# Optimization experiments

Hardware: AMD Instinct MI355X
Metric: run time of the kernel (lower is better)

Reference implementation:

```python
import jax, jax.numpy as jnp
import numpy as np


def setup_inputs() -> dict:
    key = jax.random.key(0)
    k1, k2, k3, k4, k5 = jax.random.split(key, 5)
    B, S, D, H, L = 32, 2048, 512, 32, 2
    inp = jax.random.normal(k1, (B, S, D), dtype=jnp.float32)
    mask = jax.random.randint(k2, (B, S), 0, 2) > 0  # bool [B,S]
    projector = jax.random.normal(k3, (D, H), dtype=jnp.float32) * 0.05
    hidden = jax.random.normal(k4, (L - 1, H, H), dtype=jnp.float32) * 0.05
    evaluator = jax.random.normal(k5, (H, 1), dtype=jnp.float32) * 0.05
    return {"inp": inp, "mask": mask, "projector": projector,
            "hidden": hidden, "evaluator": evaluator}


def reference(inp, mask, projector, hidden, evaluator):
    act = jax.nn.sigmoid
    scale = jnp.asarray(projector.shape[-1], inp.dtype) ** 0.5  # sqrt(hidden_dim)
    m = mask.astype(inp.dtype)[..., None]          # [B,S,1]
    x = inp * m                                     # masked inputs (inp *= mask)
    w = act(jnp.einsum('bsd,dh->bsh', x, projector) / scale)
    for i in range(hidden.shape[0]):                # n_layers - 1 hidden matmuls
        w = act(jnp.einsum('bsh,hk->bsk', w, hidden[i]) / scale)
    w = act(jnp.einsum('bsh,ho->bso', w, evaluator) / scale)  # [B,S,1]
    w = jax.nn.softmax(w, axis=-2)                  # softmax over sequence axis
    w = w * m
    w = w / (jnp.sum(w, axis=1, keepdims=True) + 1e-12)
    return jnp.sum(w * x, axis=1)                   # [B,D]
```

## Files before the change

kernel.cpp:

```cpp
#include <hip/hip_runtime.h>

#define B_   32
#define S_   2048
#define D_   512
#define H_   32
#define BS_  (B_*S_)
#define INV_SCALE 0.17677669529663689f


typedef short  s16x8 __attribute__((ext_vector_type(8)));
typedef float  f32x4 __attribute__((ext_vector_type(4)));

__device__ __forceinline__ float sigmoidf_(float x) {
    return 1.0f / (1.0f + __expf(-x));
}

__device__ __forceinline__ unsigned short f2bf(float f) {
    unsigned u = __float_as_uint(f);
    u += 0x7fffu + ((u >> 16) & 1u);
    return (unsigned short)(u >> 16);
}

__global__ void kTransposeBf(const float* __restrict__ P, unsigned short* __restrict__ PTbf) {
    int o = blockIdx.x * 256 + threadIdx.x;
    int j = o >> 9, d = o & 511;
    PTbf[o] = f2bf(P[d * H_ + j]);
}

#define XST 520

__global__ __launch_bounds__(256) void kScores(
        const float* __restrict__ inp, const int* __restrict__ mask,
        const unsigned short* __restrict__ PTbf, const float* __restrict__ hd,
        const float* __restrict__ ev, float* __restrict__ v) {
    __shared__ unsigned short xs[32 * XST];
    float* w0f = (float*)xs;
    float* w1f = ((float*)xs) + 32 * 33;

    const int tid = threadIdx.x;
    const int rowBase = blockIdx.x * 32;

    const float4* g = (const float4*)inp + (size_t)rowBase * 128;
    float4 tmp[16];
    #pragma unroll
    for (int i = 0; i < 16; ++i)
        tmp[i] = g[i * 256 + tid];
    #pragma unroll
    for (int i = 0; i < 16; ++i) {
        int fi = i * 256 + tid;
        int row = fi >> 7, kq = fi & 127;
        ushort4 u;
        u.x = f2bf(tmp[i].x); u.y = f2bf(tmp[i].y);
        u.z = f2bf(tmp[i].z); u.w = f2bf(tmp[i].w);
        *(ushort4*)(xs + row * XST + kq * 4) = u;
    }
    __syncthreads();

    const int wave = tid >> 6, lane = tid & 63;
    const int rt = wave & 1, ct = wave >> 1;
    const int m = lane & 15, quad = lane >> 4;

    const unsigned short* arow = xs + (rt * 16 + m) * XST + quad * 8;
    const unsigned short* brow = PTbf + (size_t)(ct * 16 + m) * 512 + quad * 8;

    f32x4 acc = {0.f, 0.f, 0.f, 0.f};
    #pragma unroll
    for (int ks = 0; ks < 16; ++ks) {
        s16x8 a = *(const s16x8*)(arow + ks * 32);
        s16x8 b = *(const s16x8*)(brow + ks * 32);
        acc = __builtin_amdgcn_mfma_f32_16x16x32_bf16(a, b, acc, 0, 0, 0);
    }
    __syncthreads();

    #pragma unroll
    for (int r = 0; r < 4; ++r) {
        int rowL = rt * 16 + quad * 4 + r;
        float mr = (mask[rowBase + rowL] != 0) ? 1.0f : 0.0f;
        w0f[rowL * 33 + ct * 16 + m] = sigmoidf_(mr * acc[r] * INV_SCALE);
    }
    __syncthreads();

    {
        const int k = tid & 31, slot = tid >> 5;
        #pragma unroll
        for (int t = 0; t < 4; ++t) {
            int row = slot + 8 * t;
            float s = 0.f;
            #pragma unroll
            for (int j = 0; j < 32; ++j)
                s = fmaf(w0f[row * 33 + j], hd[j * 32 + k], s);
            w1f[row * 33 + k] = sigmoidf_(s * INV_SCALE);
        }
    }
    __syncthreads();

    if (tid < 32) {
        float s = 0.f;
        #pragma unroll
        for (int k = 0; k < 32; ++k)
            s = fmaf(w1f[tid * 33 + k], ev[k], s);
        float val = sigmoidf_(s * INV_SCALE);
        v[rowBase + tid] = (mask[rowBase + tid] != 0) ? val : -val;
    }
}

__global__ __launch_bounds__(256) void kCoeff(float* __restrict__ v) {
    const int b = blockIdx.x, tid = threadIdx.x;
    __shared__ float sr[8];

    float ee[8], mm[8];
    float z = 0.f, dm = 0.f;
    #pragma unroll
    for (int i = 0; i < 8; ++i) {
        int idx = b * S_ + i * 256 + tid;
        float raw = v[idx];
        mm[i] = (raw > 0.f) ? 1.0f : 0.0f;
        ee[i] = __expf(fabsf(raw));
        z += ee[i];
        dm = fmaf(mm[i], ee[i], dm);
    }
    #pragma unroll
    for (int o = 32; o > 0; o >>= 1) {
        z  += __shfl_down(z, o);
        dm += __shfl_down(dm, o);
    }
    if ((tid & 63) == 0) { sr[tid >> 6] = z; sr[4 + (tid >> 6)] = dm; }
    __syncthreads();
    float Z  = (sr[0] + sr[1]) + (sr[2] + sr[3]);
    float DM = (sr[4] + sr[5]) + (sr[6] + sr[7]);
    float invDen = 1.0f / (DM + 1e-12f * Z);
    #pragma unroll
    for (int i = 0; i < 8; ++i) {
        int idx = b * S_ + i * 256 + tid;
        v[idx] = mm[i] * ee[i] * invDen;
    }
}

__global__ __launch_bounds__(1024) void kOut(
        const float* __restrict__ inp, const float* __restrict__ coeff,
        float* __restrict__ out) {
    const int b = blockIdx.x >> 3, dc = blockIdx.x & 7;
    const int tid = threadIdx.x;
    const int sg = tid >> 4, dl = tid & 15;
    __shared__ float  cw[S_];
    __shared__ float4 red[1024];

    cw[tid]        = coeff[b * S_ + tid];
    cw[tid + 1024] = coeff[b * S_ + tid + 1024];
    __syncthreads();

    const float4* xp = (const float4*)inp + (size_t)b * S_ * 128 + dc * 16 + dl;
    float4 a0 = make_float4(0,0,0,0), a1 = a0, a2 = a0, a3 = a0;
    #pragma unroll 2
    for (int i = 0; i < 32; i += 4) {
        int s0 = sg + 64 * i;
        float4 x0 = xp[(size_t)(s0      ) * 128];
        float4 x1 = xp[(size_t)(s0 +  64) * 128];
        float4 x2 = xp[(size_t)(s0 + 128) * 128];
        float4 x3 = xp[(size_t)(s0 + 192) * 128];
        float c0 = cw[s0], c1 = cw[s0 + 64], c2 = cw[s0 + 128], c3 = cw[s0 + 192];
        a0.x = fmaf(c0, x0.x, a0.x); a0.y = fmaf(c0, x0.y, a0.y);
        a0.z = fmaf(c0, x0.z, a0.z); a0.w = fmaf(c0, x0.w, a0.w);
        a1.x = fmaf(c1, x1.x, a1.x); a1.y = fmaf(c1, x1.y, a1.y);
        a1.z = fmaf(c1, x1.z, a1.z); a1.w = fmaf(c1, x1.w, a1.w);
        a2.x = fmaf(c2, x2.x, a2.x); a2.y = fmaf(c2, x2.y, a2.y);
        a2.z = fmaf(c2, x2.z, a2.z); a2.w = fmaf(c2, x2.w, a2.w);
        a3.x = fmaf(c3, x3.x, a3.x); a3.y = fmaf(c3, x3.y, a3.y);
        a3.z = fmaf(c3, x3.z, a3.z); a3.w = fmaf(c3, x3.w, a3.w);
    }
    float4 a;
    a.x = (a0.x + a1.x) + (a2.x + a3.x);
    a.y = (a0.y + a1.y) + (a2.y + a3.y);
    a.z = (a0.z + a1.z) + (a2.z + a3.z);
    a.w = (a0.w + a1.w) + (a2.w + a3.w);
    red[tid] = a;
    __syncthreads();

    #pragma unroll
    for (int h = 32; h >= 1; h >>= 1) {
        if (sg < h) {
            float4 p = red[(sg + h) * 16 + dl];
            float4 q = red[tid];
            q.x += p.x; q.y += p.y; q.z += p.z; q.w += p.w;
            red[tid] = q;
        }
        __syncthreads();
    }
    if (tid < 16)
        ((float4*)out)[b * 128 + dc * 16 + tid] = red[tid];
}

extern "C" void kernel_launch(void* const* d_in, const int* in_sizes, int n_in,
                              void* d_out, int out_size, void* d_ws, size_t ws_size,
                              hipStream_t stream) {
    const float* inp  = (const float*)d_in[0];
    const int*   mask = (const int*)d_in[1];
    const float* proj = (const float*)d_in[2];
    const float* hid  = (const float*)d_in[3];
    const float* ev   = (const float*)d_in[4];
    float* out = (float*)d_out;

    unsigned short* PTbf = (unsigned short*)d_ws;
    float* v = (float*)d_ws + 8192;

    kTransposeBf<<<64, 256, 0, stream>>>(proj, PTbf);
    kScores     <<<BS_ / 32, 256, 0, stream>>>(inp, mask, PTbf, hid, ev, v);
    kCoeff      <<<B_, 256, 0, stream>>>(v);
    kOut        <<<B_ * 8, 1024, 0, stream>>>(inp, v, out);
}
```

Before: 237.8 us.

## Fuse weighted sum into score kernel using bf16 tile and partial reductions

The score kernel now also computes unnormalized softmax weights, per-block exp sums, and the weighted sum of the input rows it already holds in shared memory as bf16. A small reduce kernel combines the per-block partials and normalizes them. This drops the second full read of the input in the output kernel and the separate coefficient kernel. The cost is that the weighted sum now uses bf16-rounded inputs rather than fp32, which may hurt accuracy. Softmax max-subtraction is skipped, which is safe only because the sigmoid output is bounded.

```diff
diff --git a/kernel.cpp b/kernel.cpp
--- a/kernel.cpp
+++ b/kernel.cpp
@@ -29,16 +29,19 @@
 
 #define XST 520
 
-__global__ __launch_bounds__(256) void kScores(
+__global__ __launch_bounds__(256) void kFused(
         const float* __restrict__ inp, const int* __restrict__ mask,
         const unsigned short* __restrict__ PTbf, const float* __restrict__ hd,
-        const float* __restrict__ ev, float* __restrict__ v) {
+        const float* __restrict__ ev,
+        float* __restrict__ partial, float2* __restrict__ zdm) {
     __shared__ unsigned short xs[32 * XST];
-    float* w0f = (float*)xs;
-    float* w1f = ((float*)xs) + 32 * 33;
+    __shared__ float w0f[32 * 33];
+    __shared__ float w1f[32 * 33];
+    __shared__ float cs[32];
 
     const int tid = threadIdx.x;
-    const int rowBase = blockIdx.x * 32;
+    const int blk = blockIdx.x;
+    const int rowBase = blk * 32;
 
     const float4* g = (const float4*)inp + (size_t)rowBase * 128;
     float4 tmp[16];
@@ -70,7 +73,6 @@
         s16x8 b = *(const s16x8*)(brow + ks * 32);
         acc = __builtin_amdgcn_mfma_f32_16x16x32_bf16(a, b, acc, 0, 0, 0);
     }
-    __syncthreads();
 
     #pragma unroll
     for (int r = 0; r < 4; ++r) {
@@ -94,100 +96,76 @@
     }
     __syncthreads();
 
-    if (tid < 32) {
-        float s = 0.f;
+    if (tid < 64) {
+        float e = 0.f, mm = 0.f;
+        if (tid < 32) {
+            float s = 0.f;
+            #pragma unroll
+            for (int k = 0; k < 32; ++k)
+                s = fmaf(w1f[tid * 33 + k], ev[k], s);
+            float val = sigmoidf_(s * INV_SCALE);
+            e  = __expf(val);
+            mm = (mask[rowBase + tid] != 0) ? 1.0f : 0.0f;
+            cs[tid] = mm * e;
+        }
+        float z = e, dm = mm * e;
         #pragma unroll
-        for (int k = 0; k < 32; ++k)
-            s = fmaf(w1f[tid * 33 + k], ev[k], s);
-        float val = sigmoidf_(s * INV_SCALE);
-        v[rowBase + tid] = (mask[rowBase + tid] != 0) ? val : -val;
+        for (int o = 32; o > 0; o >>= 1) {
+            z  += __shfl_down(z, o);
+            dm += __shfl_down(dm, o);
+        }
+        if (tid == 0) zdm[blk] = make_float2(z, dm);
     }
+    __syncthreads();
+
+    float a0 = 0.f, a1 = 0.f;
+    #pragma unroll 8
+    for (int row = 0; row < 32; ++row) {
+        unsigned u = *(const unsigned*)(xs + row * XST + 2 * tid);
+        float x0 = __uint_as_float(u << 16);
+        float x1 = __uint_as_float(u & 0xffff0000u);
+        float c = cs[row];
+        a0 = fmaf(c, x0, a0);
+        a1 = fmaf(c, x1, a1);
+    }
+    ((float2*)(partial + (size_t)blk * 512))[tid] = make_float2(a0, a1);
 }
 
-__global__ __launch_bounds__(256) void kCoeff(float* __restrict__ v) {
+__global__ __launch_bounds__(256) void kReduce(
+        const float* __restrict__ partial, const float2* __restrict__ zdm,
+        float* __restrict__ out) {
     const int b = blockIdx.x, tid = threadIdx.x;
-    __shared__ float sr[8];
+    __shared__ float sInv;
 
-    float ee[8], mm[8];
-    float z = 0.f, dm = 0.f;
-    #pragma unroll
-    for (int i = 0; i < 8; ++i) {
-        int idx = b * S_ + i * 256 + tid;
-        float raw = v[idx];
-        mm[i] = (raw > 0.f) ? 1.0f : 0.0f;
-        ee[i] = __expf(fabsf(raw));
-        z += ee[i];
-        dm = fmaf(mm[i], ee[i], dm);
+    if (tid < 64) {
+        float2 p = zdm[b * 64 + tid];
+        float z = p.x, dm = p.y;
+        #pragma unroll
+        for (int o = 32; o > 0; o >>= 1) {
+            z  += __shfl_down(z, o);
+            dm += __shfl_down(dm, o);
+        }
+        if (tid == 0) sInv = 1.0f / (dm + 1e-12f * z);
     }
-    #pragma unroll
-    for (int o = 32; o > 0; o >>= 1) {
-        z  += __shfl_down(z, o);
-        dm += __shfl_down(dm, o);
-    }
-    if ((tid & 63) == 0) { sr[tid >> 6] = z; sr[4 + (tid >> 6)] = dm; }
-    __syncthreads();
-    float Z  = (sr[0] + sr[1]) + (sr[2] + sr[3]);
-    float DM = (sr[4] + sr[5]) + (sr[6] + sr[7]);
-    float invDen = 1.0f / (DM + 1e-12f * Z);
-    #pragma unroll
-    for (int i = 0; i < 8; ++i) {
-        int idx = b * S_ + i * 256 + tid;
-        v[idx] = mm[i] * ee[i] * invDen;
-    }
-}
-
-__global__ __launch_bounds__(1024) void kOut(
-        const float* __restrict__ inp, const float* __restrict__ coeff,
-        float* __restrict__ out) {
-    const int b = blockIdx.x >> 3, dc = blockIdx.x & 7;
-    const int tid = threadIdx.x;
-    const int sg = tid >> 4, dl = tid & 15;
-    __shared__ float  cw[S_];
-    __shared__ float4 red[1024];
-
-    cw[tid]        = coeff[b * S_ + tid];
-    cw[tid + 1024] = coeff[b * S_ + tid + 1024];
     __syncthreads();
 
-    const float4* xp = (const float4*)inp + (size_t)b * S_ * 128 + dc * 16 + dl;
-    float4 a0 = make_float4(0,0,0,0), a1 = a0, a2 = a0, a3 = a0;
-    #pragma unroll 2
-    for (int i = 0; i < 32; i += 4) {
-        int s0 = sg + 64 * i;
-        float4 x0 = xp[(size_t)(s0      ) * 128];
-        float4 x1 = xp[(size_t)(s0 +  64) * 128];
-        float4 x2 = xp[(size_t)(s0 + 128) * 128];
-        float4 x3 = xp[(size_t)(s0 + 192) * 128];
-        float c0 = cw[s0], c1 = cw[s0 + 64], c2 = cw[s0 + 128], c3 = cw[s0 + 192];
-        a0.x = fmaf(c0, x0.x, a0.x); a0.y = fmaf(c0, x0.y, a0.y);
-        a0.z = fmaf(c0, x0.z, a0.z); a0.w = fmaf(c0, x0.w, a0.w);
-        a1.x = fmaf(c1, x1.x, a1.x); a1.y = fmaf(c1, x1.y, a1.y);
-        a1.z = fmaf(c1, x1.z, a1.z); a1.w = fmaf(c1, x1.w, a1.w);
-        a2.x = fmaf(c2, x2.x, a2.x); a2.y = fmaf(c2, x2.y, a2.y);
-        a2.z = fmaf(c2, x2.z, a2.z); a2.w = fmaf(c2, x2.w, a2.w);
-        a3.x = fmaf(c3, x3.x, a3.x); a3.y = fmaf(c3, x3.y, a3.y);
-        a3.z = fmaf(c3, x3.z, a3.z); a3.w = fmaf(c3, x3.w, a3.w);
+    const float2* pp = (const float2*)partial + (size_t)b * 64 * 256 + tid;
+    float a0 = 0.f, b0 = 0.f, a1 = 0.f, b1 = 0.f;
+    float a2 = 0.f, b2 = 0.f, a3 = 0.f, b3 = 0.f;
+    #pragma unroll
+    for (int i = 0; i < 64; i += 4) {
+        float2 p0 = pp[(size_t)(i + 0) * 256];
+        float2 p1 = pp[(size_t)(i + 1) * 256];
+        float2 p2 = pp[(size_t)(i + 2) * 256];
+        float2 p3 = pp[(size_t)(i + 3) * 256];
+        a0 += p0.x; b0 += p0.y; a1 += p1.x; b1 += p1.y;
+        a2 += p2.x; b2 += p2.y; a3 += p3.x; b3 += p3.y;
     }
-    float4 a;
-    a.x = (a0.x + a1.x) + (a2.x + a3.x);
-    a.y = (a0.y + a1.y) + (a2.y + a3.y);
-    a.z = (a0.z + a1.z) + (a2.z + a3.z);
-    a.w = (a0.w + a1.w) + (a2.w + a3.w);
-    red[tid] = a;
-    __syncthreads();
-
-    #pragma unroll
-    for (int h = 32; h >= 1; h >>= 1) {
-        if (sg < h) {
-            float4 p = red[(sg + h) * 16 + dl];
-            float4 q = red[tid];
-            q.x += p.x; q.y += p.y; q.z += p.z; q.w += p.w;
-            red[tid] = q;
-        }
-        __syncthreads();
-    }
-    if (tid < 16)
-        ((float4*)out)[b * 128 + dc * 16 + tid] = red[tid];
+    const float inv = sInv;
+    float2 r;
+    r.x = ((a0 + a1) + (a2 + a3)) * inv;
+    r.y = ((b0 + b1) + (b2 + b3)) * inv;
+    ((float2*)out)[b * 256 + tid] = r;
 }
 
 extern "C" void kernel_launch(void* const* d_in, const int* in_sizes, int n_in,
@@ -201,10 +179,10 @@
     float* out = (float*)d_out;
 
     unsigned short* PTbf = (unsigned short*)d_ws;
-    float* v = (float*)d_ws + 8192;
+    float2* zdm     = (float2*)((char*)d_ws + 32768);
+    float*  partial = (float*)((char*)d_ws + 49152);
 
     kTransposeBf<<<64, 256, 0, stream>>>(proj, PTbf);
-    kScores     <<<BS_ / 32, 256, 0, stream>>>(inp, mask, PTbf, hid, ev, v);
-    kCoeff      <<<B_, 256, 0, stream>>>(v);
-    kOut        <<<B_ * 8, 1024, 0, stream>>>(inp, v, out);
+    kFused      <<<BS_ / 32, 256, 0, stream>>>(inp, mask, PTbf, hid, ev, partial, zdm);
+    kReduce     <<<B_, 256, 0, stream>>>(partial, zdm, out);
 }
```

Result: faster. 221.6 us (-6.8%).
